# Kernel tuning notes

Measured on AMD Instinct MI355X. Metric: run time of the kernel, lower is better.

Reference implementation:

```python
import jax, jax.numpy as jnp
import numpy as np

C = 64
D = C // 8  # query/key channels
B, H, W = 4, 64, 64


def setup_inputs() -> dict:
    key = jax.random.key(0)
    ks = jax.random.split(key, 8)
    x = jax.random.normal(ks[0], (B, C, H, W), dtype=jnp.float32)
    # 1x1 conv params (kernel squeezed to [out_ch, in_ch])
    sq = 1.0 / np.sqrt(C)
    Wq = jax.random.uniform(ks[1], (D, C), jnp.float32, -sq, sq)
    bq = jax.random.uniform(ks[2], (D,), jnp.float32, -sq, sq)
    Wk = jax.random.uniform(ks[3], (D, C), jnp.float32, -sq, sq)
    bk = jax.random.uniform(ks[4], (D,), jnp.float32, -sq, sq)
    Wv = jax.random.uniform(ks[5], (C, C), jnp.float32, -sq, sq)
    bv = jax.random.uniform(ks[6], (C,), jnp.float32, -sq, sq)
    # gamma is zero-initialized in the module; use a nonzero value so the
    # attention path actually contributes to the output.
    gamma = jax.random.normal(ks[7], (1,), dtype=jnp.float32)
    return {"x": x, "Wq": Wq, "bq": bq, "Wk": Wk, "bk": bk, "Wv": Wv, "bv": bv, "gamma": gamma}


def reference(x, Wq, bq, Wk, bk, Wv, bv, gamma):
    b, c, h, w = x.shape
    n = h * w
    xf = x.reshape(b, c, n)                                   # [B,C,N]
    q = jnp.einsum('dc,bcn->bdn', Wq, xf) + bq[None, :, None]  # [B,D,N]
    k = jnp.einsum('dc,bcn->bdn', Wk, xf) + bk[None, :, None]  # [B,D,N]
    v = jnp.einsum('ec,bcn->ben', Wv, xf) + bv[None, :, None]  # [B,C,N]
    energy = jnp.einsum('bdn,bdm->bnm', q, k)                  # [B,N,N] = Q^T K
    attn = jax.nn.softmax(energy, axis=-1)                     # softmax over keys m
    # out[b,c,n] = sum_m v[b,c,m] * attn[b,n,m]  (V @ attention^T in torch)
    out = jnp.einsum('bcm,bnm->bcn', v, attn).reshape(b, c, h, w)
    return gamma[0] * out + x
```

## Files before the change

### kernel.cpp

```cpp
#include <hip/hip_runtime.h>
#include <hip/hip_bf16.h>
#include <math.h>

#define BB 4
#define CC 64
#define DD 8
#define NN 4096
#define KS 16
#define KPS (NN / KS)
#define VSTR 260
#define KSTR 12
#define LOG2E 1.44269504088896340736f

typedef __attribute__((ext_vector_type(4))) short short4v;
typedef __attribute__((ext_vector_type(4))) unsigned short ushort4v;
typedef __attribute__((ext_vector_type(8))) unsigned short ushort8;
typedef __attribute__((ext_vector_type(16))) float f32x16;

#if defined(__HIP_DEVICE_COMPILE__)
  #if __has_builtin(__builtin_amdgcn_mfma_f32_32x32x8bf16_1k)
    #define MFMA32x8(A, B, C) __builtin_amdgcn_mfma_f32_32x32x8bf16_1k(A, B, C, 0, 0, 0)
  #elif __has_builtin(__builtin_amdgcn_mfma_f32_32x32x8_bf16)
    #define MFMA32x8(A, B, C) __builtin_amdgcn_mfma_f32_32x32x8_bf16(A, B, C, 0, 0, 0)
  #else
    #error "no 32x32x8 bf16 MFMA builtin in device pass"
  #endif
  #if __has_builtin(__builtin_amdgcn_exp2f)
    #define EXP2(x) __builtin_amdgcn_exp2f(x)
  #else
    #define EXP2(x) exp2f(x)
  #endif
#else
  static __device__ __host__ inline f32x16 MFMA32x8(short4v, short4v, f32x16 c) { return c; }
  #define EXP2(x) exp2f(x)
#endif

static __device__ inline short4v pack4(float a, float b, float c, float d) {
    union { short4v s; __hip_bfloat162 h[2]; } u;
    u.h[0] = __float22bfloat162_rn(make_float2(a, b));
    u.h[1] = __float22bfloat162_rn(make_float2(c, d));
    return u.s;
}
static __device__ inline unsigned packu(float lo, float hi) {
    union { __hip_bfloat162 h; unsigned u; } t;
    t.h = __float22bfloat162_rn(make_float2(lo, hi));
    return t.u;
}

__global__ __launch_bounds__(256) void qkv_kernel(
    const float* __restrict__ x,  const float* __restrict__ Wq, const float* __restrict__ bq,
    const float* __restrict__ Wk, const float* __restrict__ bk,
    const float* __restrict__ Wv, const float* __restrict__ bv,
    unsigned short* __restrict__ qb, unsigned short* __restrict__ kb,
    unsigned short* __restrict__ vT)
{
    __shared__ unsigned short LQ[128 * 8];
    __shared__ unsigned short LK[128 * 8];

    int tid = threadIdx.x;
    int wave = tid >> 6, lane = tid & 63;
    int l32 = lane & 31, h2 = lane >> 5;

    int blk = blockIdx.x;
    int b = blk & (BB - 1);
    int r2 = blk >> 2;
    int rt = r2 % 3;
    int ng = r2 / 3;
    int n0 = ng * 128 + wave * 32;

    short4v af[8];
    #pragma unroll
    for (int s = 0; s < 8; ++s) {
        float4 w4;
        if (rt < 2) {
            w4 = *(const float4*)(Wv + (size_t)(rt * 32 + l32) * CC + s * 8 + 4 * h2);
        } else if (l32 < 8) {
            w4 = *(const float4*)(Wq + (size_t)l32 * CC + s * 8 + 4 * h2);
        } else if (l32 < 16) {
            w4 = *(const float4*)(Wk + (size_t)(l32 - 8) * CC + s * 8 + 4 * h2);
        } else {
            w4 = make_float4(0.f, 0.f, 0.f, 0.f);
        }
        af[s] = pack4(w4.x, w4.y, w4.z, w4.w);
    }

    const float* xb = x + (size_t)b * CC * NN + n0 + l32;
    short4v bf[8];
    #pragma unroll
    for (int s = 0; s < 8; ++s) {
        int c0 = s * 8 + 4 * h2;
        float x0 = xb[(size_t)(c0 + 0) * NN];
        float x1 = xb[(size_t)(c0 + 1) * NN];
        float x2 = xb[(size_t)(c0 + 2) * NN];
        float x3 = xb[(size_t)(c0 + 3) * NN];
        bf[s] = pack4(x0, x1, x2, x3);
    }

    f32x16 acc;
    #pragma unroll
    for (int r = 0; r < 16; ++r) acc[r] = 0.f;
    #pragma unroll
    for (int s = 0; s < 8; ++s)
        acc = MFMA32x8(af[s], bf[s], acc);

    if (rt < 2) {
        #pragma unroll
        for (int r = 0; r < 16; ++r) {
            int row = rt * 32 + (r & 3) + 8 * (r >> 2) + 4 * h2;
            float val = acc[r] + bv[row];
            __hip_bfloat16 hv = __float2bfloat16(val);
            vT[((size_t)b * CC + row) * NN + n0 + l32] = *(unsigned short*)&hv;
        }
    } else {
        short4v qp = pack4((acc[0] + bq[0 + 4 * h2]) * LOG2E,
                           (acc[1] + bq[1 + 4 * h2]) * LOG2E,
                           (acc[2] + bq[2 + 4 * h2]) * LOG2E,
                           (acc[3] + bq[3 + 4 * h2]) * LOG2E);
        short4v kp = pack4(acc[4] + bk[0 + 4 * h2],
                           acc[5] + bk[1 + 4 * h2],
                           acc[6] + bk[2 + 4 * h2],
                           acc[7] + bk[3 + 4 * h2]);
        int nl = wave * 32 + l32;
        *(short4v*)(LQ + (size_t)nl * 8 + 4 * h2) = qp;
        *(short4v*)(LK + (size_t)nl * 8 + 4 * h2) = kp;
        __syncthreads();
        if (tid < 128) {
            ushort8 row = *(const ushort8*)(LQ + (size_t)tid * 8);
            *(ushort8*)(qb + ((size_t)b * NN + ng * 128 + tid) * 8) = row;
        } else {
            int t = tid - 128;
            ushort8 row = *(const ushort8*)(LK + (size_t)t * 8);
            *(ushort8*)(kb + ((size_t)b * NN + ng * 128 + t) * 8) = row;
        }
    }
}

__global__ __launch_bounds__(512, 6) void flash_kernel(
    const unsigned short* __restrict__ qb, const unsigned short* __restrict__ kb,
    const unsigned short* __restrict__ vT, unsigned* __restrict__ accb,
    float* __restrict__ sbuf)
{
    __shared__ unsigned short VS[64 * VSTR];
    __shared__ unsigned short KL[256 * KSTR];
    int tid = threadIdx.x;
    int wave = tid >> 6, lane = tid & 63;
    int l32 = lane & 31, h2 = lane >> 5;

    int blk = blockIdx.x;
    int b = blk & (BB - 1);
    int rest = blk >> 2;
    int split = rest & (KS - 1);
    int qchunk = rest >> 4;
    int n0 = qchunk * 256 + wave * 32;

    short4v qf = *(const short4v*)(qb + ((size_t)b * NN + n0 + l32) * DD + h2 * 4);

    const unsigned short* kbb = kb + (size_t)b * NN * DD;
    const unsigned short* vbb = vT + (size_t)b * CC * NN;
    int m0 = split * KPS;

    int ch = tid >> 3, ks0 = (tid & 7) * 32;
    {
        const unsigned short* vg = vbb + (size_t)ch * NN + m0 + ks0;
        ushort8 v0 = *(const ushort8*)(vg);
        ushort8 v1 = *(const ushort8*)(vg + 8);
        ushort8 v2 = *(const ushort8*)(vg + 16);
        ushort8 v3 = *(const ushort8*)(vg + 24);
        ushort8 kA = {0,0,0,0,0,0,0,0};
        if (tid < 256) kA = *(const ushort8*)(kbb + (size_t)(m0 + tid) * DD);

        unsigned short* vp = VS + (size_t)ch * VSTR + ks0;
        *(ushort4v*)(vp)      = *(ushort4v*)&v0;
        *(ushort4v*)(vp + 4)  = *((ushort4v*)&v0 + 1);
        *(ushort4v*)(vp + 8)  = *(ushort4v*)&v1;
        *(ushort4v*)(vp + 12) = *((ushort4v*)&v1 + 1);
        *(ushort4v*)(vp + 16) = *(ushort4v*)&v2;
        *(ushort4v*)(vp + 20) = *((ushort4v*)&v2 + 1);
        *(ushort4v*)(vp + 24) = *(ushort4v*)&v3;
        *(ushort4v*)(vp + 28) = *((ushort4v*)&v3 + 1);
        if (tid < 256) {
            unsigned short* p = KL + (size_t)tid * KSTR;
            *(ushort4v*)(p)     = *(ushort4v*)&kA;
            *(ushort4v*)(p + 4) = *((ushort4v*)&kA + 1);
        }
    }
    __syncthreads();

    f32x16 o0, o1, zz;
    #pragma unroll
    for (int r = 0; r < 16; ++r) { o0[r] = 0.f; o1[r] = 0.f; zz[r] = 0.f; }
    float s0 = 0.f, s1 = 0.f, s2 = 0.f, s3 = 0.f;

    #pragma unroll
    for (int s = 0; s < 8; ++s) {
        short4v kf = *(const short4v*)(KL + (size_t)(s * 32 + l32) * KSTR + h2 * 4);
        f32x16 st = MFMA32x8(kf, qf, zz);
        float w[16];
        #pragma unroll
        for (int r = 0; r < 16; ++r) w[r] = EXP2(st[r]);
        s0 += (w[0] + w[1]) + (w[2] + w[3]);
        s1 += (w[4] + w[5]) + (w[6] + w[7]);
        s2 += (w[8] + w[9]) + (w[10] + w[11]);
        s3 += (w[12] + w[13]) + (w[14] + w[15]);

        union { short4v s; __hip_bfloat162 h[2]; } u[4];
        #pragma unroll
        for (int g = 0; g < 4; ++g) {
            u[g].h[0] = __float22bfloat162_rn(make_float2(w[4 * g],     w[4 * g + 1]));
            u[g].h[1] = __float22bfloat162_rn(make_float2(w[4 * g + 2], w[4 * g + 3]));
        }
        #pragma unroll
        for (int g = 0; g < 4; ++g) {
            int gg = s * 4 + g;
            short4v vf0 = *(const short4v*)(VS + (size_t)(l32)      * VSTR + gg * 8 + h2 * 4);
            short4v vf1 = *(const short4v*)(VS + (size_t)(32 + l32) * VSTR + gg * 8 + h2 * 4);
            o0 = MFMA32x8(u[g].s, vf0, o0);
            o1 = MFMA32x8(u[g].s, vf1, o1);
        }
    }

    unsigned* au = accb + (((size_t)((b * KS + split) * 128 + qchunk * 8 + wave)) << 10);
    #pragma unroll
    for (int r = 0; r < 16; ++r)
        au[r * 64 + lane] = packu(o0[r], o1[r]);

    float ssum = (s0 + s1) + (s2 + s3);
    ssum += __shfl_xor(ssum, 32);
    if (lane < 32)
        sbuf[(size_t)(b * KS + split) * NN + n0 + l32] = ssum;
}

__global__ __launch_bounds__(256) void norm_kernel(
    const unsigned* __restrict__ accb, const float* __restrict__ sbuf,
    const float* __restrict__ x, const float* __restrict__ gamma,
    float* __restrict__ out)
{
    __shared__ float tile[16 * 65];
    __shared__ float stl[16];
    int blk = blockIdx.x;
    int b = blk >> 8;
    int h = blk & 255;
    int g32 = h >> 1;
    int qhalf = h & 1;
    int n0 = g32 * 32 + qhalf * 16;
    int tid = threadIdx.x;

    if (tid < 16) {
        float st = 0.f;
        #pragma unroll
        for (int sp = 0; sp < KS; ++sp)
            st += sbuf[(size_t)(b * KS + sp) * NN + n0 + tid];
        stl[tid] = 1.0f / st;
    }

    int spoff = tid >> 7;
    int u = tid & 127;
    int rl = u >> 4;
    int lane0 = (u & 15) * 4;

    float alo[4], ahi[4];
    #pragma unroll
    for (int e = 0; e < 4; ++e) { alo[e] = 0.f; ahi[e] = 0.f; }
    #pragma unroll
    for (int p = 0; p < 8; ++p) {
        int sp = p * 2 + spoff;
        const unsigned* base = accb + (((size_t)((b * KS + sp) * 128 + g32)) << 10)
                             + qhalf * 512;
        uint4 v = *(const uint4*)(base + u * 4);
        unsigned wv[4] = {v.x, v.y, v.z, v.w};
        #pragma unroll
        for (int e = 0; e < 4; ++e) {
            alo[e] += __uint_as_float(wv[e] << 16);
            ahi[e] += __uint_as_float(wv[e] & 0xFFFF0000u);
        }
    }

    #pragma unroll
    for (int e = 0; e < 4; ++e) {
        int lane = lane0 + e;
        int h2 = lane >> 5, l32 = lane & 31;
        int ql = (rl & 3) + 8 * ((rl >> 2) & 1) + 4 * h2;
        if (tid < 128) {
            tile[ql * 65 + l32]      = alo[e];
            tile[ql * 65 + 32 + l32] = ahi[e];
        }
    }
    __syncthreads();
    #pragma unroll
    for (int e = 0; e < 4; ++e) {
        int lane = lane0 + e;
        int h2 = lane >> 5, l32 = lane & 31;
        int ql = (rl & 3) + 8 * ((rl >> 2) & 1) + 4 * h2;
        if (tid >= 128) {
            tile[ql * 65 + l32]      += alo[e];
            tile[ql * 65 + 32 + l32] += ahi[e];
        }
    }
    __syncthreads();

    float gm = gamma[0];
    #pragma unroll
    for (int p2 = 0; p2 < 4; ++p2) {
        int idx = p2 * 256 + tid;
        int c = idx >> 4, ql = idx & 15;
        size_t xi = ((size_t)b * CC + c) * NN + n0 + ql;
        out[xi] = gm * tile[ql * 65 + c] * stl[ql] + x[xi];
    }
}

extern "C" void kernel_launch(void* const* d_in, const int* in_sizes, int n_in,
                              void* d_out, int out_size, void* d_ws, size_t ws_size,
                              hipStream_t stream)
{
    const float* x     = (const float*)d_in[0];
    const float* Wq    = (const float*)d_in[1];
    const float* bq    = (const float*)d_in[2];
    const float* Wk    = (const float*)d_in[3];
    const float* bk    = (const float*)d_in[4];
    const float* Wv    = (const float*)d_in[5];
    const float* bv    = (const float*)d_in[6];
    const float* gamma = (const float*)d_in[7];
    float* out = (float*)d_out;

    float* ws = (float*)d_ws;
    size_t off = 0;
    unsigned short* qb = (unsigned short*)(ws + off); off += (size_t)BB * NN * DD / 2 + 64;
    unsigned short* kb = (unsigned short*)(ws + off); off += (size_t)BB * NN * DD / 2 + 64;
    unsigned short* vT = (unsigned short*)(ws + off); off += (size_t)BB * CC * NN / 2 + 64;
    unsigned* accb = (unsigned*)(ws + off); off += (size_t)BB * KS * NN * CC / 2;
    float* sbuf = ws + off; off += (size_t)BB * KS * NN;

    qkv_kernel<<<BB * 3 * 32, 256, 0, stream>>>(x, Wq, bq, Wk, bk, Wv, bv, qb, kb, vT);
    flash_kernel<<<BB * 16 * KS, 512, 0, stream>>>(qb, kb, vT, accb, sbuf);
    norm_kernel<<<BB * 256, 256, 0, stream>>>(accb, sbuf, x, gamma, out);
}
```

Measured before the change: 102.5 us.

## Halve key splits and use 32x32x16 bf16 MFMA for PV product

Reduces the number of key splits from 16 to 8, so each flash block processes 512 keys with larger LDS tiles for V and K. The PV accumulation is switched from pairs of 32x32x8 MFMAs to the 32x32x16 bf16 instruction where available, assembling 8-wide operands from two LDS reads. The point is to cut partial-accumulator traffic and reduction work in the norm kernel and to issue fewer MFMAs. In exchange it launches half as many blocks, uses more LDS per block, and lowers the occupancy hint.

```diff
diff --git a/kernel.cpp b/kernel.cpp
--- a/kernel.cpp
+++ b/kernel.cpp
@@ -6,13 +6,14 @@
 #define CC 64
 #define DD 8
 #define NN 4096
-#define KS 16
+#define KS 8
 #define KPS (NN / KS)
-#define VSTR 260
+#define VSTR 516
 #define KSTR 12
 #define LOG2E 1.44269504088896340736f
 
 typedef __attribute__((ext_vector_type(4))) short short4v;
+typedef __attribute__((ext_vector_type(8))) short short8s;
 typedef __attribute__((ext_vector_type(4))) unsigned short ushort4v;
 typedef __attribute__((ext_vector_type(8))) unsigned short ushort8;
 typedef __attribute__((ext_vector_type(16))) float f32x16;
@@ -34,6 +35,18 @@
   static __device__ __host__ inline f32x16 MFMA32x8(short4v, short4v, f32x16 c) { return c; }
   #define EXP2(x) exp2f(x)
 #endif
+
+static __device__ inline f32x16 PVMFMA(short8s A, short8s B, f32x16 c) {
+#if defined(__HIP_DEVICE_COMPILE__) && __has_builtin(__builtin_amdgcn_mfma_f32_32x32x16_bf16)
+    typedef __attribute__((ext_vector_type(8))) __bf16 bf16x8;
+    return __builtin_amdgcn_mfma_f32_32x32x16_bf16(
+        __builtin_bit_cast(bf16x8, A), __builtin_bit_cast(bf16x8, B), c, 0, 0, 0);
+#else
+    union { short8s v; short4v h[2]; } a, b;
+    a.v = A; b.v = B;
+    return MFMA32x8(a.h[1], b.h[1], MFMA32x8(a.h[0], b.h[0], c));
+#endif
+}
 
 static __device__ inline short4v pack4(float a, float b, float c, float d) {
     union { short4v s; __hip_bfloat162 h[2]; } u;
@@ -135,13 +148,13 @@
     }
 }
 
-__global__ __launch_bounds__(512, 6) void flash_kernel(
+__global__ __launch_bounds__(512, 4) void flash_kernel(
     const unsigned short* __restrict__ qb, const unsigned short* __restrict__ kb,
     const unsigned short* __restrict__ vT, unsigned* __restrict__ accb,
     float* __restrict__ sbuf)
 {
     __shared__ unsigned short VS[64 * VSTR];
-    __shared__ unsigned short KL[256 * KSTR];
+    __shared__ unsigned short KL[512 * KSTR];
     int tid = threadIdx.x;
     int wave = tid >> 6, lane = tid & 63;
     int l32 = lane & 31, h2 = lane >> 5;
@@ -150,7 +163,7 @@
     int b = blk & (BB - 1);
     int rest = blk >> 2;
     int split = rest & (KS - 1);
-    int qchunk = rest >> 4;
+    int qchunk = rest >> 3;
     int n0 = qchunk * 256 + wave * 32;
 
     short4v qf = *(const short4v*)(qb + ((size_t)b * NN + n0 + l32) * DD + h2 * 4);
@@ -159,30 +172,23 @@
     const unsigned short* vbb = vT + (size_t)b * CC * NN;
     int m0 = split * KPS;
 
-    int ch = tid >> 3, ks0 = (tid & 7) * 32;
     {
-        const unsigned short* vg = vbb + (size_t)ch * NN + m0 + ks0;
-        ushort8 v0 = *(const ushort8*)(vg);
-        ushort8 v1 = *(const ushort8*)(vg + 8);
-        ushort8 v2 = *(const ushort8*)(vg + 16);
-        ushort8 v3 = *(const ushort8*)(vg + 24);
-        ushort8 kA = {0,0,0,0,0,0,0,0};
-        if (tid < 256) kA = *(const ushort8*)(kbb + (size_t)(m0 + tid) * DD);
-
-        unsigned short* vp = VS + (size_t)ch * VSTR + ks0;
-        *(ushort4v*)(vp)      = *(ushort4v*)&v0;
-        *(ushort4v*)(vp + 4)  = *((ushort4v*)&v0 + 1);
-        *(ushort4v*)(vp + 8)  = *(ushort4v*)&v1;
-        *(ushort4v*)(vp + 12) = *((ushort4v*)&v1 + 1);
-        *(ushort4v*)(vp + 16) = *(ushort4v*)&v2;
-        *(ushort4v*)(vp + 20) = *((ushort4v*)&v2 + 1);
-        *(ushort4v*)(vp + 24) = *(ushort4v*)&v3;
-        *(ushort4v*)(vp + 28) = *((ushort4v*)&v3 + 1);
-        if (tid < 256) {
-            unsigned short* p = KL + (size_t)tid * KSTR;
-            *(ushort4v*)(p)     = *(ushort4v*)&kA;
-            *(ushort4v*)(p + 4) = *((ushort4v*)&kA + 1);
-        }
+        int ch = tid >> 3, s8 = (tid & 7) * 8;
+        const unsigned short* vg = vbb + (size_t)ch * NN + m0 + s8;
+        ushort8 v[8];
+        #pragma unroll
+        for (int k = 0; k < 8; ++k) v[k] = *(const ushort8*)(vg + 64 * k);
+        ushort8 kA = *(const ushort8*)(kbb + (size_t)(m0 + tid) * DD);
+
+        unsigned short* vp = VS + (size_t)ch * VSTR + s8;
+        #pragma unroll
+        for (int k = 0; k < 8; ++k) {
+            *(ushort4v*)(vp + 64 * k)     = *(ushort4v*)&v[k];
+            *(ushort4v*)(vp + 64 * k + 4) = *((ushort4v*)&v[k] + 1);
+        }
+        unsigned short* p = KL + (size_t)tid * KSTR;
+        *(ushort4v*)(p)     = *(ushort4v*)&kA;
+        *(ushort4v*)(p + 4) = *((ushort4v*)&kA + 1);
     }
     __syncthreads();
 
@@ -192,7 +198,7 @@
     float s0 = 0.f, s1 = 0.f, s2 = 0.f, s3 = 0.f;
 
     #pragma unroll
-    for (int s = 0; s < 8; ++s) {
+    for (int s = 0; s < 16; ++s) {
         short4v kf = *(const short4v*)(KL + (size_t)(s * 32 + l32) * KSTR + h2 * 4);
         f32x16 st = MFMA32x8(kf, qf, zz);
         float w[16];
@@ -210,12 +216,17 @@
             u[g].h[1] = __float22bfloat162_rn(make_float2(w[4 * g + 2], w[4 * g + 3]));
         }
         #pragma unroll
-        for (int g = 0; g < 4; ++g) {
-            int gg = s * 4 + g;
-            short4v vf0 = *(const short4v*)(VS + (size_t)(l32)      * VSTR + gg * 8 + h2 * 4);
-            short4v vf1 = *(const short4v*)(VS + (size_t)(32 + l32) * VSTR + gg * 8 + h2 * 4);
-            o0 = MFMA32x8(u[g].s, vf0, o0);
-            o1 = MFMA32x8(u[g].s, vf1, o1);
+        for (int j = 0; j < 2; ++j) {
+            int kb0 = s * 32 + j * 16 + h2 * 4;
+            union { short8s v; short4v h[2]; } A, B0, B1;
+            A.h[0] = u[2 * j].s;
+            A.h[1] = u[2 * j + 1].s;
+            B0.h[0] = *(const short4v*)(VS + (size_t)(l32)      * VSTR + kb0);
+            B0.h[1] = *(const short4v*)(VS + (size_t)(l32)      * VSTR + kb0 + 8);
+            B1.h[0] = *(const short4v*)(VS + (size_t)(32 + l32) * VSTR + kb0);
+            B1.h[1] = *(const short4v*)(VS + (size_t)(32 + l32) * VSTR + kb0 + 8);
+            o0 = PVMFMA(A.v, B0.v, o0);
+            o1 = PVMFMA(A.v, B1.v, o1);
         }
     }
 
@@ -262,7 +273,7 @@
     #pragma unroll
     for (int e = 0; e < 4; ++e) { alo[e] = 0.f; ahi[e] = 0.f; }
     #pragma unroll
-    for (int p = 0; p < 8; ++p) {
+    for (int p = 0; p < 4; ++p) {
         int sp = p * 2 + spoff;
         const unsigned* base = accb + (((size_t)((b * KS + sp) * 128 + g32)) << 10)
                              + qhalf * 512;
```

Result: faster. 96.37 us (-6.0%).
